# Optimization experiments

Measured on AMD Instinct MI355X. Metric: run time of the kernel, lower is better.

## Reference

```python
import jax, jax.numpy as jnp
import numpy as np

B, T, C = 32, 512, 1024
H, D = 16, 64
BLOCK_SIZE = 512


def setup_inputs() -> dict:
    key = jax.random.key(0)
    ks = jax.random.split(key, 6)
    s_in = 1.0 / np.sqrt(C)
    return {
        "x": jax.random.normal(ks[0], (B, T, C), dtype=jnp.float32),
        "wq": jax.random.normal(ks[1], (H, C, D), dtype=jnp.float32) * s_in,
        "wk": jax.random.normal(ks[2], (H, C, D), dtype=jnp.float32) * s_in,
        "wv": jax.random.normal(ks[3], (H, C, D), dtype=jnp.float32) * s_in,
        "w_proj": jax.random.normal(ks[4], (C, C), dtype=jnp.float32) * s_in,
        "b_proj": jax.random.normal(ks[5], (C,), dtype=jnp.float32) * 0.01,
    }


def reference(x, wq, wk, wv, w_proj, b_proj):
    b, t, c = x.shape
    # per-head projections (bias=False Linears stacked on head axis)
    q = jnp.einsum("btc,hcd->bhtd", x, wq)
    k = jnp.einsum("btc,hcd->bhtd", x, wk)
    v = jnp.einsum("btc,hcd->bhtd", x, wv)
    # NOTE: original scales by 1/sqrt(C) with C = n_embd, not head_size
    scale = 1.0 / (c ** 0.5)
    scores = jnp.einsum("bhtd,bhsd->bhts", q, k) * scale  # [B,H,T,T]
    causal = jnp.tril(jnp.ones((t, t), dtype=bool))
    scores = jnp.where(causal, scores, jnp.finfo(scores.dtype).min)
    attn = jax.nn.softmax(scores, axis=-1)
    out = jnp.einsum("bhts,bhsd->bhtd", attn, v)
    # concat heads in order -> [B,T,H*D]
    out = out.transpose(0, 2, 1, 3).reshape(b, t, -1)
    # output projection (dropout = identity in eval mode)
    return out @ w_proj + b_proj
```

## Files before the change

kernel.cpp:

```cpp
#include <hip/hip_runtime.h>

typedef unsigned int u32;
typedef unsigned short u16;
typedef __bf16 bf16x8 __attribute__((ext_vector_type(8)));
typedef float f32x4 __attribute__((ext_vector_type(4)));
typedef u16 u16x8 __attribute__((ext_vector_type(8)));
typedef u16 u16x4 __attribute__((ext_vector_type(4)));

#define DEVI static __device__ __forceinline__

DEVI u16 f2bf(float f) {
  union { float f; u32 u; } v; v.f = f;
  return (u16)((v.u + 0x7fffu + ((v.u >> 16) & 1u)) >> 16);
}

DEVI u32 cvtpk(float a, float b) {
  u32 r;
  asm("v_cvt_pk_bf16_f32 %0, %1, %2" : "=v"(r) : "v"(a), "v"(b));
  return r;
}

constexpr long QS_ = 16777216;
constexpr long XB_O    = 0;
constexpr long WQKV_O  = 16777216;
constexpr long Q_O     = 19922944;
constexpr long CTX_O   = 70254592;
constexpr long WPROJ_O = 87031808;

#define SCL_Q 0.045084220027780106f

__global__ __launch_bounds__(256) void k_prep_all(const float* __restrict__ x,
                                                  const float* __restrict__ wq,
                                                  const float* __restrict__ wk,
                                                  const float* __restrict__ wv,
                                                  const float* __restrict__ wp,
                                                  u16* __restrict__ ws) {
  __shared__ float tile[64][65];
  const int b = blockIdx.x;
  const int tid = threadIdx.x;
  if (b < 1024) {
    const float* src;
    u16* dst;
    long srs;
    if (b < 768) {
      int sel = b >> 8, rest = b & 255, h = rest >> 4, kt = rest & 15;
      const float* W = (sel == 0) ? wq : ((sel == 1) ? wk : wv);
      src = W + (long)(h * 1024 + kt * 64) * 64;
      srs = 64;
      dst = ws + WQKV_O + (long)(sel * 1024 + h * 64) * 1024 + kt * 64;
    } else {
      int b3 = b - 768, ntile = b3 >> 4, kt = b3 & 15;
      src = wp + (long)(kt * 64) * 1024 + ntile * 64;
      srs = 1024;
      dst = ws + WPROJ_O + (long)(ntile * 64) * 1024 + kt * 64;
    }
    #pragma unroll
    for (int i = 0; i < 4; ++i) {
      int idx = i * 256 + tid, r = idx >> 4, c4 = idx & 15;
      float4 v = *(const float4*)(src + (long)r * srs + c4 * 4);
      tile[r][c4 * 4 + 0] = v.x; tile[r][c4 * 4 + 1] = v.y;
      tile[r][c4 * 4 + 2] = v.z; tile[r][c4 * 4 + 3] = v.w;
    }
    __syncthreads();
    #pragma unroll
    for (int i = 0; i < 2; ++i) {
      int idx = i * 256 + tid, dr = idx >> 3, c8 = idx & 7;
      u16x8 o8;
      #pragma unroll
      for (int j = 0; j < 8; ++j) o8[j] = f2bf(tile[c8 * 8 + j][dr]);
      *(u16x8*)(dst + (long)dr * 1024 + c8 * 8) = o8;
    }
  } else {
    long id = (long)(b - 1024) * 256 + tid;
    const float4* p = (const float4*)(x + id * 8);
    float4 a = p[0], c = p[1];
    u16x8 r;
    r[0]=f2bf(a.x); r[1]=f2bf(a.y); r[2]=f2bf(a.z); r[3]=f2bf(a.w);
    r[4]=f2bf(c.x); r[5]=f2bf(c.y); r[6]=f2bf(c.z); r[7]=f2bf(c.w);
    *(u16x8*)(ws + XB_O + id * 8) = r;
  }
}

DEVI void gload16(const u16* g, u16* l) {
  __builtin_amdgcn_global_load_lds((const __attribute__((address_space(1))) u32*)g,
                                   (__attribute__((address_space(3))) u32*)l, 16, 0, 0);
}

template <int NN, int EPI>
__global__ __launch_bounds__(512, 2)
void k_gemm(const u16* __restrict__ A, const u16* __restrict__ Bt,
            u16* __restrict__ oq, float* __restrict__ of, const float* __restrict__ bias) {
  __shared__ u16 lds[2][4][8192];

  const int tid = threadIdx.x;
  const int lane = tid & 63;
  const int w = tid >> 6;
  const int wm = w >> 2, wn = w & 3;
  const int lg = lane >> 4, lr = lane & 15;
  const int bht = 2 + (wn >> 1);
  const int bn0 = (wn & 1) * 4;

  constexpr int NBN = NN / 256;
  const int nwg = gridDim.x;
  const int swz = ((int)blockIdx.x & 7) * (nwg >> 3) + ((int)blockIdx.x >> 3);
  const long m0 = (long)(swz / NBN) * 256, n0 = (long)(swz % NBN) * 256;

  int srcoff[2];
  #pragma unroll
  for (int r2 = 0; r2 < 2; ++r2) {
    int s = r2 * 8 + w;
    int mi = s >> 1, ks = s & 1;
    int rowl = mi * 16 + (lane >> 2);
    int colu = ks * 32 + (((lane & 3) * 8) ^ (((lane >> 5) & 1) * 16));
    srcoff[r2] = rowl * 1024 + colu;
  }
  const int fo = lr * 32 + ((lg * 8) ^ (((lr >> 3) & 1) * 16));

  const u16* At  = A  + m0 * 1024;
  const u16* Bt2 = Bt + n0 * 1024;

  f32x4 acc[8][4] = {};
  bf16x8 aq[2][2][2];
  bf16x8 bfr[4][2];

#define STAGE(buf_, ht_, gbase_)                                               \
  { _Pragma("unroll") for (int r_ = 0; r_ < 2; ++r_)                           \
      gload16((gbase_) + srcoff[r_], &lds[buf_][ht_][r_ * 4096 + w * 512]); }

#define LDS_AQ(set_, buf_, q_)                                                 \
  { _Pragma("unroll") for (int i_ = 0; i_ < 2; ++i_)                           \
    _Pragma("unroll") for (int ks_ = 0; ks_ < 2; ++ks_)                        \
      aq[set_][i_][ks_] = *(const bf16x8*)&lds[buf_][wm][(((q_)*2 + i_) * 2 + ks_) * 512 + fo]; }

#define LDS_BF(buf_, lo_)                                                      \
  { _Pragma("unroll") for (int j_ = 0; j_ < 2; ++j_)                           \
    _Pragma("unroll") for (int ks_ = 0; ks_ < 2; ++ks_)                        \
      bfr[(lo_) + j_][ks_] = *(const bf16x8*)&lds[buf_][bht][((bn0 + (lo_) + j_) * 2 + ks_) * 512 + fo]; }

#define QUAD8(set_, q_, lo_)                                                   \
  { __builtin_amdgcn_s_setprio(1);                                             \
    _Pragma("unroll") for (int ks_ = 0; ks_ < 2; ++ks_)                        \
    _Pragma("unroll") for (int i_ = 0; i_ < 2; ++i_)                           \
    _Pragma("unroll") for (int j_ = 0; j_ < 2; ++j_)                           \
      acc[(q_)*2 + i_][(lo_) + j_] = __builtin_amdgcn_mfma_f32_16x16x32_bf16(  \
          aq[set_][i_][ks_], bfr[(lo_) + j_][ks_], acc[(q_)*2 + i_][(lo_) + j_], 0, 0, 0); \
    __builtin_amdgcn_s_setprio(0); }

#define BARF() { asm volatile("s_barrier" ::: "memory"); }

  STAGE(0, 0, At);
  STAGE(0, 1, At + 131072);
  STAGE(0, 2, Bt2);
  STAGE(0, 3, Bt2 + 131072);
  STAGE(1, 0, At + 64);
  STAGE(1, 1, At + 131072 + 64);
  STAGE(1, 2, Bt2 + 64);
  STAGE(1, 3, Bt2 + 131072 + 64);
  asm volatile("s_waitcnt vmcnt(8)" ::: "memory");
  BARF();
  LDS_AQ(0, 0, 0);
  LDS_BF(0, 0);

  #pragma unroll 1
  for (int t = 0; t < 16; ++t) {
    const int buf = t & 1;
    LDS_BF(buf, 2);
    LDS_AQ(1, buf, 1);
    QUAD8(0, 0, 0);
    BARF();
    QUAD8(0, 0, 2);
    BARF();
    LDS_AQ(0, buf, 2);
    if (t + 2 < 16) { STAGE(buf, 2, Bt2 + (t + 2) * 64); STAGE(buf, 3, Bt2 + 131072 + (t + 2) * 64); }
    QUAD8(1, 1, 0);
    BARF();
    QUAD8(1, 1, 2);
    BARF();
    LDS_AQ(1, buf, 3);
    QUAD8(0, 2, 0);
    BARF();
    QUAD8(0, 2, 2);
    asm volatile("s_waitcnt lgkmcnt(0)" ::: "memory");
    __builtin_amdgcn_sched_barrier(0);
    BARF();
    if (t + 2 < 16) { STAGE(buf, 0, At + (t + 2) * 64); STAGE(buf, 1, At + 131072 + (t + 2) * 64); }
    QUAD8(1, 3, 0);
    BARF();
    if (t < 14)       { asm volatile("s_waitcnt vmcnt(8)" ::: "memory"); }
    else if (t == 14) { asm volatile("s_waitcnt vmcnt(0)" ::: "memory"); }
    BARF();
    if (t + 1 < 16) {
      LDS_AQ(0, buf ^ 1, 0);
      LDS_BF(buf ^ 1, 0);
    }
    QUAD8(1, 3, 2);
    BARF();
  }

  if constexpr (EPI == 0) {
    #pragma unroll
    for (int mi = 0; mi < 8; ++mi) {
      int grow = (int)m0 + wm * 128 + mi * 16 + lg * 4;
      int b = grow >> 9, t0 = grow & 511;
      #pragma unroll
      for (int ni = 0; ni < 4; ++ni) {
        int gcol = (int)n0 + wn * 64 + ni * 16 + lr;
        int sel = gcol >> 10, h = (gcol >> 6) & 15, d = gcol & 63;
        float scl = (sel == 0) ? SCL_Q : 1.0f;
        u16* dst = oq + (long)sel * QS_ + (((long)(b * 16 + h) * 512 + t0) * 64 + d);
        #pragma unroll
        for (int r = 0; r < 4; ++r) dst[r * 64] = f2bf(acc[mi][ni][r] * scl);
      }
    }
  } else {
    float bv[4];
    #pragma unroll
    for (int ni = 0; ni < 4; ++ni) bv[ni] = bias[(int)n0 + wn * 64 + ni * 16 + lr];
    #pragma unroll
    for (int mi = 0; mi < 8; ++mi) {
      int grow = (int)m0 + wm * 128 + mi * 16 + lg * 4;
      #pragma unroll
      for (int ni = 0; ni < 4; ++ni) {
        int gcol = (int)n0 + wn * 64 + ni * 16 + lr;
        #pragma unroll
        for (int r = 0; r < 4; ++r)
          of[(long)(grow + r) * NN + gcol] = acc[mi][ni][r] + bv[ni];
      }
    }
  }
#undef STAGE
#undef LDS_AQ
#undef LDS_BF
#undef QUAD8
#undef BARF
}

__global__ __launch_bounds__(256, 3)
void k_attn(const u16* __restrict__ Qp, const u16* __restrict__ Kp,
            const u16* __restrict__ Vp, u16* __restrict__ ctx) {
  __shared__ u16 k_lds[2][64 * 72];
  __shared__ u16 vt_lds[2][64 * 72];

  const int bid = blockIdx.x;
  const int qi = 3 - (bid >> 9);
  const int bh = bid & 511;
  const int tid = threadIdx.x, lane = tid & 63, w = tid >> 6;
  const int lg = lane >> 4, lr = lane & 15;
  const long base = (long)bh * (512 * 64);

  const int q0 = qi * 128 + w * 32;

  bf16x8 qf[2][2];
  #pragma unroll
  for (int mt = 0; mt < 2; ++mt)
    #pragma unroll
    for (int k2 = 0; k2 < 2; ++k2)
      qf[mt][k2] = *(const bf16x8*)(Qp + base + (long)(q0 + mt * 16 + lr) * 64 + k2 * 32 + lg * 8);

  f32x4 o[2][4] = {};
  float ls[2] = {0.f, 0.f};
  u32 pkw[2][4][2];

  const int nch = (qi + 1) * 2;
  int srow[2], scol[2], cslot[2];
  #pragma unroll
  for (int i = 0; i < 2; ++i) {
    int s = i * 256 + tid;
    srow[i] = s >> 3; scol[i] = s & 7;
    int sr = srow[i];
    cslot[i] = ((sr >> 5) << 5) + (((sr >> 2) & 3) << 3) + (((sr >> 4) & 1) << 2) + (sr & 3);
  }

  uint4 kreg[2], vreg[2];
  auto loadch = [&](int c) {
    #pragma unroll
    for (int i = 0; i < 2; ++i) {
      long go = base + (long)(c * 64 + srow[i]) * 64 + scol[i] * 8;
      kreg[i] = *(const uint4*)(Kp + go);
      vreg[i] = *(const uint4*)(Vp + go);
    }
  };
  auto writech = [&](int bsel) {
    #pragma unroll
    for (int i = 0; i < 2; ++i) {
      *(uint4*)&k_lds[bsel][srow[i] * 72 + scol[i] * 8] = kreg[i];
      union { uint4 v; u16 s[8]; } t; t.v = vreg[i];
      #pragma unroll
      for (int j = 0; j < 8; ++j)
        vt_lds[bsel][(scol[i] * 8 + j) * 72 + cslot[i]] = t.s[j];
    }
  };
  auto pv_step = [&](int vsel) {
    bf16x8 vf2[4][2];
    #pragma unroll
    for (int dt = 0; dt < 4; ++dt)
      #pragma unroll
      for (int k2 = 0; k2 < 2; ++k2)
        vf2[dt][k2] = *(const bf16x8*)&vt_lds[vsel][(dt * 16 + lr) * 72 + k2 * 32 + lg * 8];
    __builtin_amdgcn_s_setprio(1);
    #pragma unroll
    for (int k2 = 0; k2 < 2; ++k2)
      #pragma unroll
      for (int mt = 0; mt < 2; ++mt) {
        union { u32 w4[4]; bf16x8 v; } pb;
        pb.w4[0] = pkw[mt][2 * k2][0];
        pb.w4[1] = pkw[mt][2 * k2][1];
        pb.w4[2] = pkw[mt][2 * k2 + 1][0];
        pb.w4[3] = pkw[mt][2 * k2 + 1][1];
        #pragma unroll
        for (int dt = 0; dt < 4; ++dt)
          o[mt][dt] = __builtin_amdgcn_mfma_f32_16x16x32_bf16(vf2[dt][k2], pb.v, o[mt][dt], 0, 0, 0);
      }
    __builtin_amdgcn_s_setprio(0);
  };

  loadch(0);
  writech(0);
  loadch(1);
  __syncthreads();

  #pragma unroll 1
  for (int c = 0; c < nch; ++c) {
    const int bsel = c & 1;
    const bool doQK = (c * 64 <= q0 + 31);
    const bool doPV = (c >= 1) && ((c - 1) * 64 <= q0 + 31);

    f32x4 st[2][4] = {};
    if (doQK) {
      bf16x8 kf2[4][2];
      #pragma unroll
      for (int nt = 0; nt < 4; ++nt)
        #pragma unroll
        for (int k2 = 0; k2 < 2; ++k2)
          kf2[nt][k2] = *(const bf16x8*)&k_lds[bsel][(nt * 16 + lr) * 72 + k2 * 32 + lg * 8];
      __builtin_amdgcn_s_setprio(1);
      #pragma unroll
      for (int k2 = 0; k2 < 2; ++k2)
        #pragma unroll
        for (int mt = 0; mt < 2; ++mt)
          #pragma unroll
          for (int nt = 0; nt < 4; ++nt)
            st[mt][nt] = __builtin_amdgcn_mfma_f32_16x16x32_bf16(kf2[nt][k2], qf[mt][k2], st[mt][nt], 0, 0, 0);
      __builtin_amdgcn_s_setprio(0);
    }

    if (doPV) pv_step(bsel ^ 1);

    if (doQK) {
      const bool full = (c * 64 + 63 <= q0);
      #pragma unroll
      for (int mt = 0; mt < 2; ++mt) {
        const int q = q0 + mt * 16 + lr;
        if (!full) {
          #pragma unroll
          for (int nt = 0; nt < 4; ++nt)
            #pragma unroll
            for (int r = 0; r < 4; ++r) {
              int s_ = c * 64 + nt * 16 + lg * 4 + r;
              st[mt][nt][r] = (s_ <= q) ? st[mt][nt][r] : -1e30f;
            }
        }
        float ps = 0.f;
        float p[4][4];
        #pragma unroll
        for (int nt = 0; nt < 4; ++nt)
          #pragma unroll
          for (int r = 0; r < 4; ++r) {
            float pv = exp2f(st[mt][nt][r]);
            p[nt][r] = pv;
            ps += pv;
          }
        ls[mt] += ps;
        #pragma unroll
        for (int nt = 0; nt < 4; ++nt) {
          pkw[mt][nt][0] = cvtpk(p[nt][0], p[nt][1]);
          pkw[mt][nt][1] = cvtpk(p[nt][2], p[nt][3]);
        }
      }
    }

    __syncthreads();
    if (c + 1 < nch) writech(bsel ^ 1);
    if (c + 2 < nch) loadch(c + 2);
    __syncthreads();
  }

  if ((nch - 1) * 64 <= q0 + 31) pv_step((nch - 1) & 1);

  const int b = bh >> 4, h = bh & 15;
  #pragma unroll
  for (int mt = 0; mt < 2; ++mt) {
    float l = ls[mt];
    l += __shfl_xor(l, 16);
    l += __shfl_xor(l, 32);
    const float inv = 1.0f / l;
    const int t = q0 + mt * 16 + lr;
    #pragma unroll
    for (int dt = 0; dt < 4; ++dt) {
      u16x4 pk4;
      #pragma unroll
      for (int r = 0; r < 4; ++r) pk4[r] = f2bf(o[mt][dt][r] * inv);
      *(u16x4*)(ctx + ((long)(b * 512 + t)) * 1024 + h * 64 + dt * 16 + lg * 4) = pk4;
    }
  }
}

extern "C" void kernel_launch(void* const* d_in, const int* in_sizes, int n_in,
                              void* d_out, int out_size, void* d_ws, size_t ws_size,
                              hipStream_t stream) {
  const float* x  = (const float*)d_in[0];
  const float* wq = (const float*)d_in[1];
  const float* wk = (const float*)d_in[2];
  const float* wv = (const float*)d_in[3];
  const float* wp = (const float*)d_in[4];
  const float* bp = (const float*)d_in[5];
  float* out = (float*)d_out;
  u16* ws = (u16*)d_ws;

  u16* XB    = ws + XB_O;
  u16* WQKV  = ws + WQKV_O;
  u16* Qb    = ws + Q_O;
  u16* CTX   = ws + CTX_O;
  u16* WPROJ = ws + WPROJ_O;

  k_prep_all<<<9216, 256, 0, stream>>>(x, wq, wk, wv, wp, ws);
  k_gemm<3072, 0><<<(16384 / 256) * (3072 / 256), 512, 0, stream>>>(XB, WQKV, Qb, nullptr, nullptr);
  k_attn<<<2048, 256, 0, stream>>>(Qb, Qb + QS_, Qb + 2 * QS_, CTX);
  k_gemm<1024, 1><<<(16384 / 256) * (1024 / 256), 512, 0, stream>>>(CTX, WPROJ, nullptr, out, bp);
}
```

Baseline: 221.9 us.

## Make QKV GEMM persistent over multiple N panels and reorder attention PV/QK

The QKV GEMM now launches 256 workgroups, each computing three consecutive 256-wide N panels for one M tile. The K-loop pipeline runs continuously across panel boundaries, with an epilogue and accumulator reset after each panel. This removes the tail wave of the 768-block grid and keeps the prefetch pipeline full between panels, but it serializes each epilogue inside the loop. In attention, the K fragments are now loaded from LDS before the PV step so that the load latency overlaps the PV MFMAs, at the cost of holding more registers live.

```diff
diff --git a/kernel.cpp b/kernel.cpp
--- a/kernel.cpp
+++ b/kernel.cpp
@@ -86,7 +86,7 @@
                                    (__attribute__((address_space(3))) u32*)l, 16, 0, 0);
 }
 
-template <int NN, int EPI>
+template <int NN, int EPI, int PANELS>
 __global__ __launch_bounds__(512, 2)
 void k_gemm(const u16* __restrict__ A, const u16* __restrict__ Bt,
             u16* __restrict__ oq, float* __restrict__ of, const float* __restrict__ bias) {
@@ -100,10 +100,12 @@
   const int bht = 2 + (wn >> 1);
   const int bn0 = (wn & 1) * 4;
 
-  constexpr int NBN = NN / 256;
+  constexpr int NBG = NN / 256 / PANELS;
+  constexpr int NG = 16 * PANELS;
   const int nwg = gridDim.x;
   const int swz = ((int)blockIdx.x & 7) * (nwg >> 3) + ((int)blockIdx.x >> 3);
-  const long m0 = (long)(swz / NBN) * 256, n0 = (long)(swz % NBN) * 256;
+  const int bm = swz / NBG, bng = swz % NBG;
+  const long m0 = (long)bm * 256;
 
   int srcoff[2];
   #pragma unroll
@@ -116,8 +118,8 @@
   }
   const int fo = lr * 32 + ((lg * 8) ^ (((lr >> 3) & 1) * 16));
 
-  const u16* At  = A  + m0 * 1024;
-  const u16* Bt2 = Bt + n0 * 1024;
+  const u16* At    = A  + m0 * 1024;
+  const u16* Bbase = Bt + (long)bng * PANELS * 262144;
 
   f32x4 acc[8][4] = {};
   bf16x8 aq[2][2][2];
@@ -148,22 +150,60 @@
 
 #define BARF() { asm volatile("s_barrier" ::: "memory"); }
 
+  auto epilogue = [&](int p) {
+    const int n0 = (bng * PANELS + p) * 256;
+    if constexpr (EPI == 0) {
+      #pragma unroll
+      for (int mi = 0; mi < 8; ++mi) {
+        int grow = (int)m0 + wm * 128 + mi * 16 + lg * 4;
+        int b = grow >> 9, t0 = grow & 511;
+        #pragma unroll
+        for (int ni = 0; ni < 4; ++ni) {
+          int gcol = n0 + wn * 64 + ni * 16 + lr;
+          int sel = gcol >> 10, h = (gcol >> 6) & 15, d = gcol & 63;
+          float scl = (sel == 0) ? SCL_Q : 1.0f;
+          u16* dst = oq + (long)sel * QS_ + (((long)(b * 16 + h) * 512 + t0) * 64 + d);
+          #pragma unroll
+          for (int r = 0; r < 4; ++r) dst[r * 64] = f2bf(acc[mi][ni][r] * scl);
+        }
+      }
+    } else {
+      float bv[4];
+      #pragma unroll
+      for (int ni = 0; ni < 4; ++ni) bv[ni] = bias[n0 + wn * 64 + ni * 16 + lr];
+      #pragma unroll
+      for (int mi = 0; mi < 8; ++mi) {
+        int grow = (int)m0 + wm * 128 + mi * 16 + lg * 4;
+        #pragma unroll
+        for (int ni = 0; ni < 4; ++ni) {
+          int gcol = n0 + wn * 64 + ni * 16 + lr;
+          #pragma unroll
+          for (int r = 0; r < 4; ++r)
+            of[(long)(grow + r) * NN + gcol] = acc[mi][ni][r] + bv[ni];
+        }
+      }
+    }
+  };
+
   STAGE(0, 0, At);
   STAGE(0, 1, At + 131072);
-  STAGE(0, 2, Bt2);
-  STAGE(0, 3, Bt2 + 131072);
+  STAGE(0, 2, Bbase);
+  STAGE(0, 3, Bbase + 131072);
   STAGE(1, 0, At + 64);
   STAGE(1, 1, At + 131072 + 64);
-  STAGE(1, 2, Bt2 + 64);
-  STAGE(1, 3, Bt2 + 131072 + 64);
+  STAGE(1, 2, Bbase + 64);
+  STAGE(1, 3, Bbase + 131072 + 64);
   asm volatile("s_waitcnt vmcnt(8)" ::: "memory");
   BARF();
   LDS_AQ(0, 0, 0);
   LDS_BF(0, 0);
 
   #pragma unroll 1
-  for (int t = 0; t < 16; ++t) {
-    const int buf = t & 1;
+  for (int g = 0; g < NG; ++g) {
+    const int buf = g & 1;
+    const u16* Asrc = At + ((g + 2) & 15) * 64;
+    const u16* Bsrc = Bbase + (long)((g + 2) >> 4) * 262144 + ((g + 2) & 15) * 64;
+
     LDS_BF(buf, 2);
     LDS_AQ(1, buf, 1);
     QUAD8(0, 0, 0);
@@ -171,7 +211,7 @@
     QUAD8(0, 0, 2);
     BARF();
     LDS_AQ(0, buf, 2);
-    if (t + 2 < 16) { STAGE(buf, 2, Bt2 + (t + 2) * 64); STAGE(buf, 3, Bt2 + 131072 + (t + 2) * 64); }
+    if (g + 2 < NG) { STAGE(buf, 2, Bsrc); STAGE(buf, 3, Bsrc + 131072); }
     QUAD8(1, 1, 0);
     BARF();
     QUAD8(1, 1, 2);
@@ -183,48 +223,26 @@
     asm volatile("s_waitcnt lgkmcnt(0)" ::: "memory");
     __builtin_amdgcn_sched_barrier(0);
     BARF();
-    if (t + 2 < 16) { STAGE(buf, 0, At + (t + 2) * 64); STAGE(buf, 1, At + 131072 + (t + 2) * 64); }
+    if (g + 2 < NG) { STAGE(buf, 0, Asrc); STAGE(buf, 1, Asrc + 131072); }
     QUAD8(1, 3, 0);
     BARF();
-    if (t < 14)       { asm volatile("s_waitcnt vmcnt(8)" ::: "memory"); }
-    else if (t == 14) { asm volatile("s_waitcnt vmcnt(0)" ::: "memory"); }
-    BARF();
-    if (t + 1 < 16) {
+    if (g < NG - 2)       { asm volatile("s_waitcnt vmcnt(8)" ::: "memory"); }
+    else if (g == NG - 2) { asm volatile("s_waitcnt vmcnt(0)" ::: "memory"); }
+    BARF();
+    if (g + 1 < NG) {
       LDS_AQ(0, buf ^ 1, 0);
       LDS_BF(buf ^ 1, 0);
     }
     QUAD8(1, 3, 2);
     BARF();
-  }
-
-  if constexpr (EPI == 0) {
-    #pragma unroll
-    for (int mi = 0; mi < 8; ++mi) {
-      int grow = (int)m0 + wm * 128 + mi * 16 + lg * 4;
-      int b = grow >> 9, t0 = grow & 511;
-      #pragma unroll
-      for (int ni = 0; ni < 4; ++ni) {
-        int gcol = (int)n0 + wn * 64 + ni * 16 + lr;
-        int sel = gcol >> 10, h = (gcol >> 6) & 15, d = gcol & 63;
-        float scl = (sel == 0) ? SCL_Q : 1.0f;
-        u16* dst = oq + (long)sel * QS_ + (((long)(b * 16 + h) * 512 + t0) * 64 + d);
-        #pragma unroll
-        for (int r = 0; r < 4; ++r) dst[r * 64] = f2bf(acc[mi][ni][r] * scl);
-      }
-    }
-  } else {
-    float bv[4];
-    #pragma unroll
-    for (int ni = 0; ni < 4; ++ni) bv[ni] = bias[(int)n0 + wn * 64 + ni * 16 + lr];
-    #pragma unroll
-    for (int mi = 0; mi < 8; ++mi) {
-      int grow = (int)m0 + wm * 128 + mi * 16 + lg * 4;
-      #pragma unroll
-      for (int ni = 0; ni < 4; ++ni) {
-        int gcol = (int)n0 + wn * 64 + ni * 16 + lr;
-        #pragma unroll
-        for (int r = 0; r < 4; ++r)
-          of[(long)(grow + r) * NN + gcol] = acc[mi][ni][r] + bv[ni];
+
+    if ((g & 15) == 15) {
+      epilogue(g >> 4);
+      if (g + 1 < NG) {
+        #pragma unroll
+        for (int mi = 0; mi < 8; ++mi)
+          #pragma unroll
+          for (int ni = 0; ni < 4; ++ni) acc[mi][ni] = f32x4{0.f, 0.f, 0.f, 0.f};
       }
     }
   }
@@ -325,14 +343,19 @@
     const bool doQK = (c * 64 <= q0 + 31);
     const bool doPV = (c >= 1) && ((c - 1) * 64 <= q0 + 31);
 
+    bf16x8 kf2[4][2];
+    if (doQK) {
+      #pragma unroll
+      for (int nt = 0; nt < 4; ++nt)
+        #pragma unroll
+        for (int k2 = 0; k2 < 2; ++k2)
+          kf2[nt][k2] = *(const bf16x8*)&k_lds[bsel][(nt * 16 + lr) * 72 + k2 * 32 + lg * 8];
+    }
+
+    if (doPV) pv_step(bsel ^ 1);
+
     f32x4 st[2][4] = {};
     if (doQK) {
-      bf16x8 kf2[4][2];
-      #pragma unroll
-      for (int nt = 0; nt < 4; ++nt)
-        #pragma unroll
-        for (int k2 = 0; k2 < 2; ++k2)
-          kf2[nt][k2] = *(const bf16x8*)&k_lds[bsel][(nt * 16 + lr) * 72 + k2 * 32 + lg * 8];
       __builtin_amdgcn_s_setprio(1);
       #pragma unroll
       for (int k2 = 0; k2 < 2; ++k2)
@@ -342,11 +365,7 @@
           for (int nt = 0; nt < 4; ++nt)
             st[mt][nt] = __builtin_amdgcn_mfma_f32_16x16x32_bf16(kf2[nt][k2], qf[mt][k2], st[mt][nt], 0, 0, 0);
       __builtin_amdgcn_s_setprio(0);
-    }
-
-    if (doPV) pv_step(bsel ^ 1);
-
-    if (doQK) {
+
       const bool full = (c * 64 + 63 <= q0);
       #pragma unroll
       for (int mt = 0; mt < 2; ++mt) {
@@ -424,7 +443,7 @@
   u16* WPROJ = ws + WPROJ_O;
 
   k_prep_all<<<9216, 256, 0, stream>>>(x, wq, wk, wv, wp, ws);
-  k_gemm<3072, 0><<<(16384 / 256) * (3072 / 256), 512, 0, stream>>>(XB, WQKV, Qb, nullptr, nullptr);
+  k_gemm<3072, 0, 3><<<256, 512, 0, stream>>>(XB, WQKV, Qb, nullptr, nullptr);
   k_attn<<<2048, 256, 0, stream>>>(Qb, Qb + QS_, Qb + 2 * QS_, CTX);
-  k_gemm<1024, 1><<<(16384 / 256) * (1024 / 256), 512, 0, stream>>>(CTX, WPROJ, nullptr, out, bp);
-}
+  k_gemm<1024, 1, 1><<<256, 512, 0, stream>>>(CTX, WPROJ, nullptr, out, bp);
+}
```

After: 218.1 us (median of 2 runs). Within noise of the previous version (-1.7%).
